# Kernel tuning notes

Hardware: AMD Instinct MI355X
Metric: run time of the kernel (lower is better)

The kernel has to match this reference:

```python
import jax, jax.numpy as jnp
import numpy as np

RPN_BBOX_STD_DEV = np.array([0.1, 0.1, 0.2, 0.2], dtype=np.float32)
PRE_NMS_LIMIT = 6000
PROPOSAL_COUNT = 1000
NMS_THRESHOLD = 0.7
BATCH = 8
NUM_ANCHORS = 261888


def setup_inputs() -> dict:
    key = jax.random.key(0)
    k1, k2, k3, k4 = jax.random.split(key, 4)
    fg = jax.random.uniform(k1, (BATCH, NUM_ANCHORS), dtype=jnp.float32)
    rpn_probs = jnp.stack([1.0 - fg, fg], axis=-1)  # [B, N, 2] (bg, fg)
    rpn_bbox = jax.random.normal(k2, (BATCH, NUM_ANCHORS, 4), dtype=jnp.float32) * 0.5
    # valid normalized anchors: y_min < y_max, x_min < x_max, inside [0, 1]
    mins = jax.random.uniform(k3, (BATCH, NUM_ANCHORS, 2), minval=0.0, maxval=0.85)
    size = jax.random.uniform(k4, (BATCH, NUM_ANCHORS, 2), minval=0.02, maxval=0.15)
    anchors = jnp.concatenate([mins, mins + size], axis=-1)  # [B, N, 4]
    return {"rpn_probs": rpn_probs, "rpn_bbox": rpn_bbox, "anchors": anchors}


def apply_box_deltas(boxes, deltas):
    # boxes: [..., (y1, x1, y2, x2)], deltas: [..., (dy, dx, log(dh), log(dw))]
    h = boxes[..., 2] - boxes[..., 0]
    w = boxes[..., 3] - boxes[..., 1]
    cy = boxes[..., 0] + 0.5 * h + deltas[..., 0] * h
    cx = boxes[..., 1] + 0.5 * w + deltas[..., 1] * w
    h = h * jnp.exp(deltas[..., 2])
    w = w * jnp.exp(deltas[..., 3])
    y1 = cy - 0.5 * h
    x1 = cx - 0.5 * w
    return jnp.stack([y1, x1, y1 + h, x1 + w], axis=-1)


def pairwise_iou(boxes):
    # boxes: [N, 4] -> iou [N, N]
    y1, x1, y2, x2 = boxes[:, 0], boxes[:, 1], boxes[:, 2], boxes[:, 3]
    area = (y2 - y1) * (x2 - x1)
    ih = jnp.maximum(jnp.minimum(y2[:, None], y2[None, :]) - jnp.maximum(y1[:, None], y1[None, :]), 0.0)
    iw = jnp.maximum(jnp.minimum(x2[:, None], x2[None, :]) - jnp.maximum(x1[:, None], x1[None, :]), 0.0)
    inter = ih * iw
    union = area[:, None] + area[None, :] - inter
    return jnp.where(union > 0.0, inter / union, 0.0)


def nms_single(boxes):
    # boxes: [K, 4], already sorted by score descending (top_k sorted=True).
    # Greedy NMS: a box is suppressed if it overlaps (IoU > thresh) a kept,
    # higher-scoring box. Sequential suppression via lax.scan over rows.
    K = boxes.shape[0]
    iou = pairwise_iou(boxes)  # [K, K]
    order = jnp.arange(K)

    def step(keep, i):
        suppress = keep[i] & (iou[i] > NMS_THRESHOLD) & (order > i)
        return keep & ~suppress, None

    keep, _ = jax.lax.scan(step, jnp.ones((K,), dtype=bool), order)
    # gather kept boxes in score order, pad with zeros to PROPOSAL_COUNT
    rank = jnp.cumsum(keep) - 1
    valid = keep & (rank < PROPOSAL_COUNT)
    dest = jnp.where(valid, rank, PROPOSAL_COUNT)  # invalid rows -> scratch row
    out = jnp.zeros((PROPOSAL_COUNT + 1, 4), boxes.dtype).at[dest].set(boxes)
    return out[:PROPOSAL_COUNT]


def reference(rpn_probs, rpn_bbox, anchors):
    scores = rpn_probs[:, :, 1]  # fg prob [B, N]
    deltas = rpn_bbox * jnp.asarray(RPN_BBOX_STD_DEV).reshape(1, 1, 4)
    k = min(PRE_NMS_LIMIT, anchors.shape[1])
    top_scores, idx = jax.lax.top_k(scores, k)  # sorted descending, [B, K]
    deltas_k = jnp.take_along_axis(deltas, idx[..., None], axis=1)   # [B, K, 4]
    anchors_k = jnp.take_along_axis(anchors, idx[..., None], axis=1)  # [B, K, 4]
    boxes = jnp.clip(apply_box_deltas(anchors_k, deltas_k), 0.0, 1.0)
    proposals = jax.vmap(nms_single)(boxes)  # [B, PROPOSAL_COUNT, 4]
    return proposals
```

## Files before the change

kernel.cpp:

```cpp
#include <hip/hip_runtime.h>
#include <hip/hip_bf16.h>

typedef unsigned long long ull;

constexpr int BATCH = 8;
constexpr int NA    = 261888;
constexpr int KSEL  = 6000;
constexpr int PROP  = 1000;
constexpr int CAP   = 8192;
constexpr int NBINS = 8192;
constexpr int HB    = 16;
constexpr int NB    = (KSEL + 63) / 64;
constexpr int NWP   = 94;
constexpr int NBLK  = 94;
constexpr int NBLK2 = 47;

constexpr size_t OFF_CNT   = 0;
constexpr size_t OFF_TSEL  = 512;
constexpr size_t OFF_BOXES = 544;
constexpr size_t OFF_MASK  = 769024;
constexpr size_t OFF_DIAG  = OFF_MASK + 36096000;
constexpr size_t OFF_SUP   = OFF_DIAG + 385024;
constexpr size_t OFF_KEYS  = OFF_MASK;
constexpr size_t OFF_HIST  = OFF_MASK + 2097152;

__device__ __forceinline__ int score_bin(float s) {
  int b = (int)(s * (float)NBINS);
  if (b < 0) b = 0;
  if (b > NBINS - 1) b = NBINS - 1;
  return b;
}

__global__ __launch_bounds__(256) void hist_kernel(const float2* __restrict__ probs,
                                                   unsigned int* __restrict__ hist,
                                                   int* __restrict__ cnt,
                                                   ull* __restrict__ keys) {
  __shared__ unsigned int lh[NBINS];
  for (int i = threadIdx.x; i < NBINS; i += 256) lh[i] = 0u;
  int fb = blockIdx.y * HB + blockIdx.x;
  if (threadIdx.x == 0) cnt[fb] = 0;
  {
    ull* kp = keys + (size_t)fb * 512;
    for (int i = threadIdx.x; i < 512; i += 256) kp[i] = ~0ull;
  }
  __syncthreads();
  int b = blockIdx.y;
  const float2* p = probs + (size_t)b * NA;
  for (int a = blockIdx.x * 256 + threadIdx.x; a < NA; a += HB * 256) {
    atomicAdd(&lh[score_bin(p[a].y)], 1u);
  }
  __syncthreads();
  unsigned int* gh = hist + ((size_t)b * HB + blockIdx.x) * NBINS;
  for (int i = threadIdx.x; i < NBINS; i += 256) gh[i] = lh[i];
}

__global__ __launch_bounds__(256) void thresh_kernel(const unsigned int* __restrict__ hist,
                                                     int* __restrict__ tsel) {
  constexpr int GR = NBINS / 256;
  __shared__ unsigned int ch[NBINS];
  __shared__ unsigned int gsum[256];
  int b = blockIdx.x;
  const unsigned int* h = hist + (size_t)b * HB * NBINS;
  for (int bin = threadIdx.x; bin < NBINS; bin += 256) {
    unsigned int s = 0;
    for (int k = 0; k < HB; ++k) s += h[(size_t)k * NBINS + bin];
    ch[bin] = s;
  }
  __syncthreads();
  unsigned int s = 0;
  int g0 = threadIdx.x * GR;
  for (int i = 0; i < GR; ++i) s += ch[g0 + i];
  gsum[threadIdx.x] = s;
  __syncthreads();
  if (threadIdx.x == 0) {
    unsigned int acc = 0;
    int g = 255;
    for (; g > 0; --g) {
      if (acc + gsum[g] >= (unsigned)KSEL) break;
      acc += gsum[g];
    }
    int t = g * GR;
    for (int bin = g * GR + GR - 1; bin >= g * GR; --bin) {
      acc += ch[bin];
      if (acc >= (unsigned)KSEL) { t = bin; break; }
    }
    tsel[b] = t;
  }
}

__global__ __launch_bounds__(256) void compact_kernel(const float2* __restrict__ probs,
                                                      const int* __restrict__ tsel,
                                                      int* __restrict__ cnt,
                                                      ull* __restrict__ keys) {
  __shared__ int lcnt, lbase;
  __shared__ ull lbuf[2048];
  int b = blockIdx.y;
  int t = tsel[b];
  if (threadIdx.x == 0) lcnt = 0;
  __syncthreads();
  const float2* p = probs + (size_t)b * NA;
  for (int a = blockIdx.x * blockDim.x + threadIdx.x; a < NA; a += gridDim.x * blockDim.x) {
    float s = p[a].y;
    if (score_bin(s) >= t) {
      int pos = atomicAdd(&lcnt, 1);
      unsigned int ib = ~__float_as_uint(s);
      lbuf[pos] = ((ull)ib << 32) | (unsigned int)a;
    }
  }
  __syncthreads();
  if (threadIdx.x == 0) lbase = atomicAdd(&cnt[b * 16], lcnt);
  __syncthreads();
  int n = lcnt, base = lbase;
  ull* kb = keys + (size_t)b * CAP;
  for (int i = threadIdx.x; i < n; i += 256) {
    int pos = base + i;
    if (pos < CAP) kb[pos] = lbuf[i];
  }
}

__global__ __launch_bounds__(256) void rankscatter_kernel(const float4* __restrict__ anchors4,
                                                          const float4* __restrict__ bbox4,
                                                          const int* __restrict__ cnt,
                                                          const ull* __restrict__ keys,
                                                          float4* __restrict__ boxes4) {
#pragma clang fp contract(off)
  __shared__ ull tile[1024];
  int b = blockIdx.y;
  int n = cnt[b * 16];
  if (n > CAP) n = CAP;
  int i = blockIdx.x * 256 + threadIdx.x;
  const ull* kb = keys + (size_t)b * CAP;
  ull my = (i < CAP) ? kb[(i < n) ? i : 0] : ~0ull;
  if (i >= n) my = ~0ull;
  unsigned int r = 0;
  int ntile = (n + 1023) & ~1023;
  for (int j0 = 0; j0 < ntile; j0 += 1024) {
    for (int k = threadIdx.x; k < 1024; k += 256) tile[k] = kb[j0 + k];
    __syncthreads();
#pragma unroll 16
    for (int k = 0; k < 1024; ++k) r += (tile[k] < my) ? 1u : 0u;
    __syncthreads();
  }
  if (i >= n || r >= (unsigned)KSEL) return;
  int a = (int)(unsigned int)(my & 0xffffffffull);
  float4 anc = anchors4[(size_t)b * NA + a];
  float4 d   = bbox4[(size_t)b * NA + a];
  float h = anc.z - anc.x;
  float w = anc.w - anc.y;
  float dy = d.x * 0.1f, dx = d.y * 0.1f, dh = d.z * 0.2f, dw = d.w * 0.2f;
  float cy = (anc.x + (0.5f * h)) + (dy * h);
  float cx = (anc.y + (0.5f * w)) + (dx * w);
  float h2 = h * expf(dh);
  float w2 = w * expf(dw);
  float y1 = cy - 0.5f * h2;
  float x1 = cx - 0.5f * w2;
  float y2 = y1 + h2;
  float x2 = x1 + w2;
  y1 = fminf(fmaxf(y1, 0.f), 1.f);
  x1 = fminf(fmaxf(x1, 0.f), 1.f);
  y2 = fminf(fmaxf(y2, 0.f), 1.f);
  x2 = fminf(fmaxf(x2, 0.f), 1.f);
  boxes4[(size_t)b * KSEL + r] = make_float4(y1, x1, y2, x2);
}

__global__ __launch_bounds__(256) void mask_kernel(const float4* __restrict__ boxes4,
                                                   ull* __restrict__ mask,
                                                   ull* __restrict__ diagT,
                                                   ull* __restrict__ superT) {
#pragma clang fp contract(off)
  int cx = blockIdx.x, rb2 = blockIdx.y, b = blockIdx.z;
  int w0 = 2 * rb2;
  int cb0 = w0 + 4 * cx;
  if (cb0 >= NWP) return;
  __shared__ float4 colbox[4][64];
  __shared__ float  colca[4][64];
  __shared__ ull wtile[128][5];
  int tid = threadIdx.x, wv = tid >> 6, l = tid & 63;
  int cb = cb0 + wv;
  int rA = rb2 * 128 + l, rB = rA + 64;
  float4 zero = make_float4(0.f, 0.f, 0.f, 0.f);
  float4 boxA = (rA < KSEL) ? boxes4[(size_t)b * KSEL + rA] : zero;
  float4 boxB = (rB < KSEL) ? boxes4[(size_t)b * KSEL + rB] : zero;
  float areaA = (boxA.z - boxA.x) * (boxA.w - boxA.y);
  float areaB = (boxB.z - boxB.x) * (boxB.w - boxB.y);
  int c = cb * 64 + l;
  float4 cload = (cb < NB && c < KSEL) ? boxes4[(size_t)b * KSEL + c] : zero;
  colbox[wv][l] = cload;
  colca[wv][l] = (cload.z - cload.x) * (cload.w - cload.y);
  __syncthreads();
  ull bitsA = 0ull, bitsB = 0ull;
  if (cb < NB) {
#pragma unroll
    for (int u = 0; u < 64; ++u) {
      float4 cbx = colbox[wv][u];
      float ca = colca[wv][u];
      {
        float ih = fmaxf(fminf(boxA.z, cbx.z) - fmaxf(boxA.x, cbx.x), 0.f);
        float iw = fmaxf(fminf(boxA.w, cbx.w) - fmaxf(boxA.y, cbx.y), 0.f);
        float inter = ih * iw;
        float uni = (areaA + ca) - inter;
        float d = fmaf(-0.7f, uni, inter);
        float tt = 6e-7f * uni;
        bool keep;
        if (__builtin_fabsf(d) <= tt) keep = (inter / uni) > 0.7f;
        else keep = d > 0.f;
        if (keep) bitsA |= (1ull << u);
      }
      {
        float ih = fmaxf(fminf(boxB.z, cbx.z) - fmaxf(boxB.x, cbx.x), 0.f);
        float iw = fmaxf(fminf(boxB.w, cbx.w) - fmaxf(boxB.y, cbx.y), 0.f);
        float inter = ih * iw;
        float uni = (areaB + ca) - inter;
        float d = fmaf(-0.7f, uni, inter);
        float tt = 6e-7f * uni;
        bool keep;
        if (__builtin_fabsf(d) <= tt) keep = (inter / uni) > 0.7f;
        else keep = d > 0.f;
        if (keep) bitsB |= (1ull << u);
      }
    }
    if (cb == w0) {
      bitsA &= (l == 63) ? 0ull : (~0ull << (l + 1));
      ull colT = 0ull;
#pragma unroll
      for (int k = 0; k < 64; ++k) {
        ull bk = __ballot(((bitsA >> k) & 1ull) != 0ull);
        if (l == k) colT = bk;
      }
      diagT[((size_t)b * NBLK + w0) * 64 + l] = colT;
    }
    if (cb == w0 + 1) {
      superT[((size_t)b * NBLK + w0) * 64 + l] = bitsA;
      bitsB &= (l == 63) ? 0ull : (~0ull << (l + 1));
      ull colT = 0ull;
#pragma unroll
      for (int k = 0; k < 64; ++k) {
        ull bk = __ballot(((bitsB >> k) & 1ull) != 0ull);
        if (l == k) colT = bk;
      }
      diagT[((size_t)b * NBLK + w0 + 1) * 64 + l] = colT;
    }
    if (cb == w0 + 2) {
      superT[((size_t)b * NBLK + w0 + 1) * 64 + l] = bitsB;
    }
  }
  wtile[l][wv] = bitsA;
  wtile[l + 64][wv] = bitsB;
  __syncthreads();
  int base_row = rb2 * 128;
#pragma unroll
  for (int pass = 0; pass < 2; ++pass) {
    int idx = pass * 256 + tid;
    int rr = idx >> 2, w = idx & 3;
    int row = base_row + rr;
    if (row < KSEL && cb0 + w < NWP)
      mask[((size_t)b * KSEL + row) * NWP + cb0 + w] = wtile[rr][w];
  }
}

__global__ __launch_bounds__(256, 1) void scan_kernel(const float4* __restrict__ boxes4,
                                                      const ull* __restrict__ mask,
                                                      const ull* __restrict__ diagT,
                                                      const ull* __restrict__ superT,
                                                      float4* __restrict__ out4) {
  __shared__ ull ldiagT[NBLK * 64];
  __shared__ ull lsuper[NBLK * 64];
  __shared__ ull S[96];
  __shared__ ull S_urg;
  __shared__ int klist[2][64];
  __shared__ int skeep[1024];
  __shared__ int s_kept, s_done, s_klen[2];
  int b = blockIdx.x;
  int tid = threadIdx.x;
  int lane = tid & 63;
  const ull* mb = mask + (size_t)b * KSEL * NWP;

  const ull* dt = diagT + (size_t)b * NBLK * 64;
  const ull* st = superT + (size_t)b * NBLK * 64;
  for (int i = tid; i < NBLK * 64; i += 256) { ldiagT[i] = dt[i]; lsuper[i] = st[i]; }
  if (tid < 96) S[tid] = 0ull;
  if (tid == 0) { s_kept = 0; s_done = 0; s_klen[0] = 0; s_klen[1] = 0; S_urg = 0ull; }
  __syncthreads();

  for (int n = 0; n < NBLK; ++n) {
    if (tid < 64) {
      ull Sn = S[n] | S_urg;
      int i0 = n * 64;
      ull colT = ldiagT[i0 + lane];
      ull sd = (n + 1 < NBLK) ? lsuper[i0 + lane] : 0ull;
      int nval = KSEL - i0;
      ull valid = (nval >= 64) ? ~0ull : ((1ull << nval) - 1ull);
      ull A = ~Sn & valid;
      ull K = 0ull;
      int kept = s_kept;
      int done = 0;
      while (A) {
        int u = __builtin_ctzll(A);
        ++kept;
        K |= (1ull << u);
        if (kept >= PROP) { done = 1; break; }
        ull sup = __ballot(((colT >> u) & 1ull) != 0ull);
        A &= ~(sup | (1ull << u));
      }
      int klen = __builtin_popcountll(K);
      int kbase = kept - klen;
      if ((K >> lane) & 1ull) {
        int rank = __builtin_popcountll(K & ((1ull << lane) - 1ull));
        skeep[kbase + rank] = i0 + lane;
        klist[n & 1][rank] = i0 + lane;
      }
      int klp = (klen + 7) & ~7;
      if (klen > 0 && lane >= klen && lane < klp)
        klist[n & 1][lane] = i0 + __builtin_ctzll(K);
      unsigned ulo = (unsigned)sd, uhi = (unsigned)(sd >> 32);
      if (!((K >> lane) & 1ull)) { ulo = 0u; uhi = 0u; }
#pragma unroll
      for (int m = 1; m < 64; m <<= 1) {
        ulo |= (unsigned)__shfl_xor((int)ulo, m, 64);
        uhi |= (unsigned)__shfl_xor((int)uhi, m, 64);
      }
      if (lane == 0) {
        s_klen[n & 1] = klen;
        S_urg = (ull)ulo | ((ull)uhi << 32);
        s_kept = kept;
        if (done || n == NBLK - 1) s_done = 1;
      }
    } else {
      int prev = (n & 1) ^ 1;
      int kl = s_klen[prev];
      int w = n + 1 + (tid - 64);
      if (kl > 0 && w < NB) {
        const int* kp = klist[prev];
        ull acc = 0ull;
        int klp = (kl + 7) & ~7;
        for (int ri = 0; ri < klp; ri += 8) {
#pragma unroll
          for (int t2 = 0; t2 < 8; ++t2)
            acc |= mb[(size_t)kp[ri + t2] * NWP + w];
        }
        S[w] |= acc;
      }
    }
    __syncthreads();
    if (s_done) break;
  }

  int fin = s_kept;
  if (fin > PROP) fin = PROP;
  for (int r2 = tid; r2 < PROP; r2 += 256) {
    float4 v = make_float4(0.f, 0.f, 0.f, 0.f);
    if (r2 < fin) v = boxes4[(size_t)b * KSEL + skeep[r2]];
    out4[(size_t)b * PROP + r2] = v;
  }
}

extern "C" void kernel_launch(void* const* d_in, const int* in_sizes, int n_in,
                              void* d_out, int out_size, void* d_ws, size_t ws_size,
                              hipStream_t stream) {
  const float2* probs   = (const float2*)d_in[0];
  const float4* bbox4   = (const float4*)d_in[1];
  const float4* anchors4= (const float4*)d_in[2];
  float4* out4 = (float4*)d_out;
  char* ws = (char*)d_ws;

  int* cnt           = (int*)(ws + OFF_CNT);
  int* tsel          = (int*)(ws + OFF_TSEL);
  float4* boxes4     = (float4*)(ws + OFF_BOXES);
  ull* maskw         = (ull*)(ws + OFF_MASK);
  ull* diagT         = (ull*)(ws + OFF_DIAG);
  ull* superT        = (ull*)(ws + OFF_SUP);
  ull* keys          = (ull*)(ws + OFF_KEYS);
  unsigned int* hist = (unsigned int*)(ws + OFF_HIST);

  hipLaunchKernelGGL(hist_kernel,        dim3(HB, BATCH),      dim3(256), 0, stream, probs, hist, cnt, keys);
  hipLaunchKernelGGL(thresh_kernel,      dim3(BATCH),          dim3(256), 0, stream, hist, tsel);
  hipLaunchKernelGGL(compact_kernel,     dim3(128, BATCH),     dim3(256), 0, stream, probs, tsel, cnt, keys);
  hipLaunchKernelGGL(rankscatter_kernel, dim3(32, BATCH),      dim3(256), 0, stream, anchors4, bbox4, cnt, keys, boxes4);
  hipLaunchKernelGGL(mask_kernel,        dim3(24, NBLK2, BATCH), dim3(256), 0, stream, boxes4, maskw, diagT, superT);
  hipLaunchKernelGGL(scan_kernel,        dim3(BATCH),          dim3(256), 0, stream, boxes4, maskw, diagT, superT, out4);
}
```

Before: 331.2 us.

## Compute NMS suppression lazily for kept boxes instead of full IoU mask

Removes the full 6000x6000 IoU bitmask precompute and its large global writes. Only the diagonal and super-diagonal 64x64 blocks are still built ahead of time. The scan kernel now runs with 1024 threads and, after each block's kept rows are known, computes IoU between those kept boxes and all later column blocks on the fly, ORing the results into the suppression words. This trades the dense mask build and the scattered mask reads for recomputed IoU work inside the sequential scan. Because only kept rows are evaluated, total work drops sharply, but the critical path of the single block per image gets longer.

```diff
diff --git a/kernel.cpp b/kernel.cpp
--- a/kernel.cpp
+++ b/kernel.cpp
@@ -11,9 +11,7 @@
 constexpr int NBINS = 8192;
 constexpr int HB    = 16;
 constexpr int NB    = (KSEL + 63) / 64;
-constexpr int NWP   = 94;
 constexpr int NBLK  = 94;
-constexpr int NBLK2 = 47;
 
 constexpr size_t OFF_CNT   = 0;
 constexpr size_t OFF_TSEL  = 512;
@@ -29,6 +27,18 @@
   if (b < 0) b = 0;
   if (b > NBINS - 1) b = NBINS - 1;
   return b;
+}
+
+__device__ __forceinline__ bool iou_keep(const float4& rb, float rA,
+                                         const float4& cb, float cA) {
+  float ih = fmaxf(fminf(rb.z, cb.z) - fmaxf(rb.x, cb.x), 0.f);
+  float iw = fmaxf(fminf(rb.w, cb.w) - fmaxf(rb.y, cb.y), 0.f);
+  float inter = ih * iw;
+  float uni = (rA + cA) - inter;
+  float d = fmaf(-0.7f, uni, inter);
+  float tt = 6e-7f * uni;
+  if (__builtin_fabsf(d) <= tt) return (inter / uni) > 0.7f;
+  return d > 0.f;
 }
 
 __global__ __launch_bounds__(256) void hist_kernel(const float2* __restrict__ probs,
@@ -163,106 +173,48 @@
   boxes4[(size_t)b * KSEL + r] = make_float4(y1, x1, y2, x2);
 }
 
-__global__ __launch_bounds__(256) void mask_kernel(const float4* __restrict__ boxes4,
-                                                   ull* __restrict__ mask,
-                                                   ull* __restrict__ diagT,
-                                                   ull* __restrict__ superT) {
+__global__ __launch_bounds__(128) void dspmask_kernel(const float4* __restrict__ boxes4,
+                                                      ull* __restrict__ diagT,
+                                                      ull* __restrict__ superT) {
 #pragma clang fp contract(off)
-  int cx = blockIdx.x, rb2 = blockIdx.y, b = blockIdx.z;
-  int w0 = 2 * rb2;
-  int cb0 = w0 + 4 * cx;
-  if (cb0 >= NWP) return;
-  __shared__ float4 colbox[4][64];
-  __shared__ float  colca[4][64];
-  __shared__ ull wtile[128][5];
+  __shared__ float4 colbox[2][64];
+  __shared__ float  colca[2][64];
+  int n = blockIdx.x, b = blockIdx.y;
   int tid = threadIdx.x, wv = tid >> 6, l = tid & 63;
-  int cb = cb0 + wv;
-  int rA = rb2 * 128 + l, rB = rA + 64;
   float4 zero = make_float4(0.f, 0.f, 0.f, 0.f);
-  float4 boxA = (rA < KSEL) ? boxes4[(size_t)b * KSEL + rA] : zero;
-  float4 boxB = (rB < KSEL) ? boxes4[(size_t)b * KSEL + rB] : zero;
-  float areaA = (boxA.z - boxA.x) * (boxA.w - boxA.y);
-  float areaB = (boxB.z - boxB.x) * (boxB.w - boxB.y);
-  int c = cb * 64 + l;
-  float4 cload = (cb < NB && c < KSEL) ? boxes4[(size_t)b * KSEL + c] : zero;
-  colbox[wv][l] = cload;
-  colca[wv][l] = (cload.z - cload.x) * (cload.w - cload.y);
-  __syncthreads();
-  ull bitsA = 0ull, bitsB = 0ull;
-  if (cb < NB) {
+  int cblk = n + wv;
+  int c = cblk * 64 + l;
+  float4 cld = (c < KSEL) ? boxes4[(size_t)b * KSEL + c] : zero;
+  colbox[wv][l] = cld;
+  colca[wv][l] = (cld.z - cld.x) * (cld.w - cld.y);
+  __syncthreads();
+  int row = n * 64 + l;
+  float4 rb = (row < KSEL) ? boxes4[(size_t)b * KSEL + row] : zero;
+  float rA = (rb.z - rb.x) * (rb.w - rb.y);
+  ull bits = 0ull;
 #pragma unroll
-    for (int u = 0; u < 64; ++u) {
-      float4 cbx = colbox[wv][u];
-      float ca = colca[wv][u];
-      {
-        float ih = fmaxf(fminf(boxA.z, cbx.z) - fmaxf(boxA.x, cbx.x), 0.f);
-        float iw = fmaxf(fminf(boxA.w, cbx.w) - fmaxf(boxA.y, cbx.y), 0.f);
-        float inter = ih * iw;
-        float uni = (areaA + ca) - inter;
-        float d = fmaf(-0.7f, uni, inter);
-        float tt = 6e-7f * uni;
-        bool keep;
-        if (__builtin_fabsf(d) <= tt) keep = (inter / uni) > 0.7f;
-        else keep = d > 0.f;
-        if (keep) bitsA |= (1ull << u);
-      }
-      {
-        float ih = fmaxf(fminf(boxB.z, cbx.z) - fmaxf(boxB.x, cbx.x), 0.f);
-        float iw = fmaxf(fminf(boxB.w, cbx.w) - fmaxf(boxB.y, cbx.y), 0.f);
-        float inter = ih * iw;
-        float uni = (areaB + ca) - inter;
-        float d = fmaf(-0.7f, uni, inter);
-        float tt = 6e-7f * uni;
-        bool keep;
-        if (__builtin_fabsf(d) <= tt) keep = (inter / uni) > 0.7f;
-        else keep = d > 0.f;
-        if (keep) bitsB |= (1ull << u);
-      }
-    }
-    if (cb == w0) {
-      bitsA &= (l == 63) ? 0ull : (~0ull << (l + 1));
-      ull colT = 0ull;
+  for (int u = 0; u < 64; ++u) {
+    if (iou_keep(rb, rA, colbox[wv][u], colca[wv][u])) bits |= (1ull << u);
+  }
+  if (wv == 0) {
+    bits &= (l == 63) ? 0ull : (~0ull << (l + 1));
+    ull colT = 0ull;
 #pragma unroll
-      for (int k = 0; k < 64; ++k) {
-        ull bk = __ballot(((bitsA >> k) & 1ull) != 0ull);
-        if (l == k) colT = bk;
-      }
-      diagT[((size_t)b * NBLK + w0) * 64 + l] = colT;
-    }
-    if (cb == w0 + 1) {
-      superT[((size_t)b * NBLK + w0) * 64 + l] = bitsA;
-      bitsB &= (l == 63) ? 0ull : (~0ull << (l + 1));
-      ull colT = 0ull;
-#pragma unroll
-      for (int k = 0; k < 64; ++k) {
-        ull bk = __ballot(((bitsB >> k) & 1ull) != 0ull);
-        if (l == k) colT = bk;
-      }
-      diagT[((size_t)b * NBLK + w0 + 1) * 64 + l] = colT;
-    }
-    if (cb == w0 + 2) {
-      superT[((size_t)b * NBLK + w0 + 1) * 64 + l] = bitsB;
-    }
-  }
-  wtile[l][wv] = bitsA;
-  wtile[l + 64][wv] = bitsB;
-  __syncthreads();
-  int base_row = rb2 * 128;
-#pragma unroll
-  for (int pass = 0; pass < 2; ++pass) {
-    int idx = pass * 256 + tid;
-    int rr = idx >> 2, w = idx & 3;
-    int row = base_row + rr;
-    if (row < KSEL && cb0 + w < NWP)
-      mask[((size_t)b * KSEL + row) * NWP + cb0 + w] = wtile[rr][w];
-  }
-}
-
-__global__ __launch_bounds__(256, 1) void scan_kernel(const float4* __restrict__ boxes4,
-                                                      const ull* __restrict__ mask,
-                                                      const ull* __restrict__ diagT,
-                                                      const ull* __restrict__ superT,
-                                                      float4* __restrict__ out4) {
+    for (int k = 0; k < 64; ++k) {
+      ull bk = __ballot(((bits >> k) & 1ull) != 0ull);
+      if (l == k) colT = bk;
+    }
+    diagT[((size_t)b * NBLK + n) * 64 + l] = colT;
+  } else {
+    superT[((size_t)b * NBLK + n) * 64 + l] = bits;
+  }
+}
+
+__global__ __launch_bounds__(1024, 1) void scan_kernel(const float4* __restrict__ boxes4,
+                                                       const ull* __restrict__ diagT,
+                                                       const ull* __restrict__ superT,
+                                                       float4* __restrict__ out4) {
+#pragma clang fp contract(off)
   __shared__ ull ldiagT[NBLK * 64];
   __shared__ ull lsuper[NBLK * 64];
   __shared__ ull S[96];
@@ -273,11 +225,12 @@
   int b = blockIdx.x;
   int tid = threadIdx.x;
   int lane = tid & 63;
-  const ull* mb = mask + (size_t)b * KSEL * NWP;
+  const float4* bx = boxes4 + (size_t)b * KSEL;
+  float4 zero = make_float4(0.f, 0.f, 0.f, 0.f);
 
   const ull* dt = diagT + (size_t)b * NBLK * 64;
   const ull* st = superT + (size_t)b * NBLK * 64;
-  for (int i = tid; i < NBLK * 64; i += 256) { ldiagT[i] = dt[i]; lsuper[i] = st[i]; }
+  for (int i = tid; i < NBLK * 64; i += 1024) { ldiagT[i] = dt[i]; lsuper[i] = st[i]; }
   if (tid < 96) S[tid] = 0ull;
   if (tid == 0) { s_kept = 0; s_done = 0; s_klen[0] = 0; s_klen[1] = 0; S_urg = 0ull; }
   __syncthreads();
@@ -309,7 +262,7 @@
         skeep[kbase + rank] = i0 + lane;
         klist[n & 1][rank] = i0 + lane;
       }
-      int klp = (klen + 7) & ~7;
+      int klp = (klen + 3) & ~3;
       if (klen > 0 && lane >= klen && lane < klp)
         klist[n & 1][lane] = i0 + __builtin_ctzll(K);
       unsigned ulo = (unsigned)sd, uhi = (unsigned)(sd >> 32);
@@ -328,17 +281,64 @@
     } else {
       int prev = (n & 1) ^ 1;
       int kl = s_klen[prev];
-      int w = n + 1 + (tid - 64);
-      if (kl > 0 && w < NB) {
+      if (kl > 0) {
+        int klp4 = (kl + 3) & ~3;
+        int lt = tid - 64;
+        int wg = lt >> 4;
+        int sub = lt & 15;
+        int c0 = sub * 4;
+        int Wcnt = NB - 1 - n;
         const int* kp = klist[prev];
-        ull acc = 0ull;
-        int klp = (kl + 7) & ~7;
-        for (int ri = 0; ri < klp; ri += 8) {
+        for (int p = 0; p * 60 + wg < Wcnt; ++p) {
+          int w = n + 1 + p * 60 + wg;
+          float4 cbx0, cbx1, cbx2, cbx3;
+          int cc = w * 64 + c0;
+          cbx0 = (cc + 0 < KSEL) ? bx[cc + 0] : zero;
+          cbx1 = (cc + 1 < KSEL) ? bx[cc + 1] : zero;
+          cbx2 = (cc + 2 < KSEL) ? bx[cc + 2] : zero;
+          cbx3 = (cc + 3 < KSEL) ? bx[cc + 3] : zero;
+          float cA0 = (cbx0.z - cbx0.x) * (cbx0.w - cbx0.y);
+          float cA1 = (cbx1.z - cbx1.x) * (cbx1.w - cbx1.y);
+          float cA2 = (cbx2.z - cbx2.x) * (cbx2.w - cbx2.y);
+          float cA3 = (cbx3.z - cbx3.x) * (cbx3.w - cbx3.y);
+          ull bits = 0ull;
+          for (int j = 0; j < klp4; j += 4) {
+            float4 r0 = bx[kp[j + 0]];
+            float4 r1 = bx[kp[j + 1]];
+            float4 r2 = bx[kp[j + 2]];
+            float4 r3 = bx[kp[j + 3]];
+            float a0 = (r0.z - r0.x) * (r0.w - r0.y);
+            float a1 = (r1.z - r1.x) * (r1.w - r1.y);
+            float a2 = (r2.z - r2.x) * (r2.w - r2.y);
+            float a3 = (r3.z - r3.x) * (r3.w - r3.y);
+            ull m0 = 0, m1 = 0, m2 = 0, m3 = 0;
+            m0 |= (ull)iou_keep(r0, a0, cbx0, cA0) << 0;
+            m0 |= (ull)iou_keep(r0, a0, cbx1, cA1) << 1;
+            m0 |= (ull)iou_keep(r0, a0, cbx2, cA2) << 2;
+            m0 |= (ull)iou_keep(r0, a0, cbx3, cA3) << 3;
+            m1 |= (ull)iou_keep(r1, a1, cbx0, cA0) << 0;
+            m1 |= (ull)iou_keep(r1, a1, cbx1, cA1) << 1;
+            m1 |= (ull)iou_keep(r1, a1, cbx2, cA2) << 2;
+            m1 |= (ull)iou_keep(r1, a1, cbx3, cA3) << 3;
+            m2 |= (ull)iou_keep(r2, a2, cbx0, cA0) << 0;
+            m2 |= (ull)iou_keep(r2, a2, cbx1, cA1) << 1;
+            m2 |= (ull)iou_keep(r2, a2, cbx2, cA2) << 2;
+            m2 |= (ull)iou_keep(r2, a2, cbx3, cA3) << 3;
+            m3 |= (ull)iou_keep(r3, a3, cbx0, cA0) << 0;
+            m3 |= (ull)iou_keep(r3, a3, cbx1, cA1) << 1;
+            m3 |= (ull)iou_keep(r3, a3, cbx2, cA2) << 2;
+            m3 |= (ull)iou_keep(r3, a3, cbx3, cA3) << 3;
+            bits |= (m0 | m1) | (m2 | m3);
+          }
+          bits <<= c0;
+          unsigned lo = (unsigned)bits, hi = (unsigned)(bits >> 32);
 #pragma unroll
-          for (int t2 = 0; t2 < 8; ++t2)
-            acc |= mb[(size_t)kp[ri + t2] * NWP + w];
+          for (int m = 1; m < 16; m <<= 1) {
+            lo |= (unsigned)__shfl_xor((int)lo, m, 64);
+            hi |= (unsigned)__shfl_xor((int)hi, m, 64);
+          }
+          if (sub == 0) S[w] |= (ull)lo | ((ull)hi << 32);
         }
-        S[w] |= acc;
       }
     }
     __syncthreads();
@@ -347,9 +347,9 @@
 
   int fin = s_kept;
   if (fin > PROP) fin = PROP;
-  for (int r2 = tid; r2 < PROP; r2 += 256) {
+  for (int r2 = tid; r2 < PROP; r2 += 1024) {
     float4 v = make_float4(0.f, 0.f, 0.f, 0.f);
-    if (r2 < fin) v = boxes4[(size_t)b * KSEL + skeep[r2]];
+    if (r2 < fin) v = bx[skeep[r2]];
     out4[(size_t)b * PROP + r2] = v;
   }
 }
@@ -366,16 +366,15 @@
   int* cnt           = (int*)(ws + OFF_CNT);
   int* tsel          = (int*)(ws + OFF_TSEL);
   float4* boxes4     = (float4*)(ws + OFF_BOXES);
-  ull* maskw         = (ull*)(ws + OFF_MASK);
   ull* diagT         = (ull*)(ws + OFF_DIAG);
   ull* superT        = (ull*)(ws + OFF_SUP);
   ull* keys          = (ull*)(ws + OFF_KEYS);
   unsigned int* hist = (unsigned int*)(ws + OFF_HIST);
 
-  hipLaunchKernelGGL(hist_kernel,        dim3(HB, BATCH),      dim3(256), 0, stream, probs, hist, cnt, keys);
-  hipLaunchKernelGGL(thresh_kernel,      dim3(BATCH),          dim3(256), 0, stream, hist, tsel);
-  hipLaunchKernelGGL(compact_kernel,     dim3(128, BATCH),     dim3(256), 0, stream, probs, tsel, cnt, keys);
-  hipLaunchKernelGGL(rankscatter_kernel, dim3(32, BATCH),      dim3(256), 0, stream, anchors4, bbox4, cnt, keys, boxes4);
-  hipLaunchKernelGGL(mask_kernel,        dim3(24, NBLK2, BATCH), dim3(256), 0, stream, boxes4, maskw, diagT, superT);
-  hipLaunchKernelGGL(scan_kernel,        dim3(BATCH),          dim3(256), 0, stream, boxes4, maskw, diagT, superT, out4);
-}
+  hipLaunchKernelGGL(hist_kernel,        dim3(HB, BATCH),    dim3(256),  0, stream, probs, hist, cnt, keys);
+  hipLaunchKernelGGL(thresh_kernel,      dim3(BATCH),        dim3(256),  0, stream, hist, tsel);
+  hipLaunchKernelGGL(compact_kernel,     dim3(128, BATCH),   dim3(256),  0, stream, probs, tsel, cnt, keys);
+  hipLaunchKernelGGL(rankscatter_kernel, dim3(32, BATCH),    dim3(256),  0, stream, anchors4, bbox4, cnt, keys, boxes4);
+  hipLaunchKernelGGL(dspmask_kernel,     dim3(NBLK, BATCH),  dim3(128),  0, stream, boxes4, diagT, superT);
+  hipLaunchKernelGGL(scan_kernel,        dim3(BATCH),        dim3(1024), 0, stream, boxes4, diagT, superT, out4);
+}
```

Result: slower. 917.9 us (+177.2%).

## Vectorize score loads as float4 and split scan mask-OR across 8 threads per word

Applied to the files above, without the earlier changes.

The histogram and compaction kernels now read two anchors' (bg, fg) probability pairs per float4 load, halving the number of load instructions over the score array. The scan kernel grows from 256 to 1024 threads, so each future suppression word is reduced by 8 threads. Each thread ORs a slice of the kept-row list and merges its result into shared memory with atomicOr. This targets the serial per-block latency of the single-block-per-image NMS scan, at the cost of shared-memory atomics and a larger block whose barriers are more expensive.

```diff
diff --git a/kernel.cpp b/kernel.cpp
--- a/kernel.cpp
+++ b/kernel.cpp
@@ -31,7 +31,7 @@
   return b;
 }
 
-__global__ __launch_bounds__(256) void hist_kernel(const float2* __restrict__ probs,
+__global__ __launch_bounds__(256) void hist_kernel(const float4* __restrict__ probs4,
                                                    unsigned int* __restrict__ hist,
                                                    int* __restrict__ cnt,
                                                    ull* __restrict__ keys) {
@@ -45,9 +45,11 @@
   }
   __syncthreads();
   int b = blockIdx.y;
-  const float2* p = probs + (size_t)b * NA;
-  for (int a = blockIdx.x * 256 + threadIdx.x; a < NA; a += HB * 256) {
-    atomicAdd(&lh[score_bin(p[a].y)], 1u);
+  const float4* p = probs4 + (size_t)b * (NA / 2);
+  for (int a = blockIdx.x * 256 + threadIdx.x; a < NA / 2; a += HB * 256) {
+    float4 v = p[a];
+    atomicAdd(&lh[score_bin(v.y)], 1u);
+    atomicAdd(&lh[score_bin(v.w)], 1u);
   }
   __syncthreads();
   unsigned int* gh = hist + ((size_t)b * HB + blockIdx.x) * NBINS;
@@ -88,7 +90,7 @@
   }
 }
 
-__global__ __launch_bounds__(256) void compact_kernel(const float2* __restrict__ probs,
+__global__ __launch_bounds__(256) void compact_kernel(const float4* __restrict__ probs4,
                                                       const int* __restrict__ tsel,
                                                       int* __restrict__ cnt,
                                                       ull* __restrict__ keys) {
@@ -98,13 +100,18 @@
   int t = tsel[b];
   if (threadIdx.x == 0) lcnt = 0;
   __syncthreads();
-  const float2* p = probs + (size_t)b * NA;
-  for (int a = blockIdx.x * blockDim.x + threadIdx.x; a < NA; a += gridDim.x * blockDim.x) {
-    float s = p[a].y;
-    if (score_bin(s) >= t) {
+  const float4* p = probs4 + (size_t)b * (NA / 2);
+  for (int a = blockIdx.x * blockDim.x + threadIdx.x; a < NA / 2; a += gridDim.x * blockDim.x) {
+    float4 v = p[a];
+    if (score_bin(v.y) >= t) {
       int pos = atomicAdd(&lcnt, 1);
-      unsigned int ib = ~__float_as_uint(s);
-      lbuf[pos] = ((ull)ib << 32) | (unsigned int)a;
+      unsigned int ib = ~__float_as_uint(v.y);
+      lbuf[pos] = ((ull)ib << 32) | (unsigned int)(2 * a);
+    }
+    if (score_bin(v.w) >= t) {
+      int pos = atomicAdd(&lcnt, 1);
+      unsigned int ib = ~__float_as_uint(v.w);
+      lbuf[pos] = ((ull)ib << 32) | (unsigned int)(2 * a + 1);
     }
   }
   __syncthreads();
@@ -258,11 +265,11 @@
   }
 }
 
-__global__ __launch_bounds__(256, 1) void scan_kernel(const float4* __restrict__ boxes4,
-                                                      const ull* __restrict__ mask,
-                                                      const ull* __restrict__ diagT,
-                                                      const ull* __restrict__ superT,
-                                                      float4* __restrict__ out4) {
+__global__ __launch_bounds__(1024, 1) void scan_kernel(const float4* __restrict__ boxes4,
+                                                       const ull* __restrict__ mask,
+                                                       const ull* __restrict__ diagT,
+                                                       const ull* __restrict__ superT,
+                                                       float4* __restrict__ out4) {
   __shared__ ull ldiagT[NBLK * 64];
   __shared__ ull lsuper[NBLK * 64];
   __shared__ ull S[96];
@@ -277,7 +284,7 @@
 
   const ull* dt = diagT + (size_t)b * NBLK * 64;
   const ull* st = superT + (size_t)b * NBLK * 64;
-  for (int i = tid; i < NBLK * 64; i += 256) { ldiagT[i] = dt[i]; lsuper[i] = st[i]; }
+  for (int i = tid; i < NBLK * 64; i += 1024) { ldiagT[i] = dt[i]; lsuper[i] = st[i]; }
   if (tid < 96) S[tid] = 0ull;
   if (tid == 0) { s_kept = 0; s_done = 0; s_klen[0] = 0; s_klen[1] = 0; S_urg = 0ull; }
   __syncthreads();
@@ -328,17 +335,20 @@
     } else {
       int prev = (n & 1) ^ 1;
       int kl = s_klen[prev];
-      int w = n + 1 + (tid - 64);
+      int lt = tid - 64;
+      int wi = lt >> 3;
+      int sub = lt & 7;
+      int w = n + 1 + wi;
       if (kl > 0 && w < NB) {
         const int* kp = klist[prev];
+        int klp8 = (kl + 7) & ~7;
+        int per = klp8 >> 3;
+        int base = sub * per;
         ull acc = 0ull;
-        int klp = (kl + 7) & ~7;
-        for (int ri = 0; ri < klp; ri += 8) {
-#pragma unroll
-          for (int t2 = 0; t2 < 8; ++t2)
-            acc |= mb[(size_t)kp[ri + t2] * NWP + w];
-        }
-        S[w] |= acc;
+#pragma unroll 8
+        for (int ri = 0; ri < per; ++ri)
+          acc |= mb[(size_t)kp[base + ri] * NWP + w];
+        if (acc) atomicOr(&S[w], acc);
       }
     }
     __syncthreads();
@@ -347,9 +357,10 @@
 
   int fin = s_kept;
   if (fin > PROP) fin = PROP;
-  for (int r2 = tid; r2 < PROP; r2 += 256) {
+  const float4* bx = boxes4 + (size_t)b * KSEL;
+  for (int r2 = tid; r2 < PROP; r2 += 1024) {
     float4 v = make_float4(0.f, 0.f, 0.f, 0.f);
-    if (r2 < fin) v = boxes4[(size_t)b * KSEL + skeep[r2]];
+    if (r2 < fin) v = bx[skeep[r2]];
     out4[(size_t)b * PROP + r2] = v;
   }
 }
@@ -357,7 +368,7 @@
 extern "C" void kernel_launch(void* const* d_in, const int* in_sizes, int n_in,
                               void* d_out, int out_size, void* d_ws, size_t ws_size,
                               hipStream_t stream) {
-  const float2* probs   = (const float2*)d_in[0];
+  const float4* probs4  = (const float4*)d_in[0];
   const float4* bbox4   = (const float4*)d_in[1];
   const float4* anchors4= (const float4*)d_in[2];
   float4* out4 = (float4*)d_out;
@@ -372,10 +383,10 @@
   ull* keys          = (ull*)(ws + OFF_KEYS);
   unsigned int* hist = (unsigned int*)(ws + OFF_HIST);
 
-  hipLaunchKernelGGL(hist_kernel,        dim3(HB, BATCH),      dim3(256), 0, stream, probs, hist, cnt, keys);
-  hipLaunchKernelGGL(thresh_kernel,      dim3(BATCH),          dim3(256), 0, stream, hist, tsel);
-  hipLaunchKernelGGL(compact_kernel,     dim3(128, BATCH),     dim3(256), 0, stream, probs, tsel, cnt, keys);
-  hipLaunchKernelGGL(rankscatter_kernel, dim3(32, BATCH),      dim3(256), 0, stream, anchors4, bbox4, cnt, keys, boxes4);
+  hipLaunchKernelGGL(hist_kernel,        dim3(HB, BATCH),      dim3(256),  0, stream, probs4, hist, cnt, keys);
+  hipLaunchKernelGGL(thresh_kernel,      dim3(BATCH),          dim3(256),  0, stream, hist, tsel);
+  hipLaunchKernelGGL(compact_kernel,     dim3(128, BATCH),     dim3(256),  0, stream, probs4, tsel, cnt, keys);
+  hipLaunchKernelGGL(rankscatter_kernel, dim3(32, BATCH),      dim3(256),  0, stream, anchors4, bbox4, cnt, keys, boxes4);
   hipLaunchKernelGGL(mask_kernel,        dim3(24, NBLK2, BATCH), dim3(256), 0, stream, boxes4, maskw, diagT, superT);
-  hipLaunchKernelGGL(scan_kernel,        dim3(BATCH),          dim3(256), 0, stream, boxes4, maskw, diagT, superT, out4);
-}
+  hipLaunchKernelGGL(scan_kernel,        dim3(BATCH),          dim3(1024), 0, stream, boxes4, maskw, diagT, superT, out4);
+}
```

Result: no change. 325.1 us (-1.8%).
